# Optimization experiments

Hardware: AMD Instinct MI355X
Metric: run time of the kernel (lower is better)

## Reference

```python
import jax, jax.numpy as jnp
import numpy as np
import math

ALPHAS = [0.5, 1.0]
LSTM_SIZE = 512
LSTM_LAYERS = 2
OUTPUT_SIZE = 1024
INPUT_SIZE = 250


def _inv_gamma(z):
    # 1/gamma(z); gamma has poles at non-positive integers -> 1/gamma = 0 (matches scipy: gamma(0)=inf)
    if z <= 0 and float(z) == int(z):
        return 0.0
    return 1.0 / math.gamma(z)


def _caputo(x, alpha):
    # x: (B, T, N). D[t] = coef * sum_{j<t} (x[t]-x[j]) * (t-j+1e-6)^(-alpha)
    T = x.shape[1]
    t = jnp.arange(T, dtype=jnp.float32)
    diff = t[:, None] - t[None, :]
    W = jnp.where(diff > 0, (jnp.abs(diff) + 1e-6) ** (-alpha), 0.0)  # (T, T) strictly lower triangular
    coef = _inv_gamma(1.0 - alpha)
    rowsum = W.sum(axis=1)  # (T,)
    # coef * (x[t] * sum_j W[t,j] - sum_j W[t,j] x[j])
    return coef * (x * rowsum[None, :, None] - jnp.einsum('tj,bjn->btn', W, x))


def _lstm_layer(x, Wih, Whh, bih, bhh):
    # x: (B, T, F); torch LSTM gate order i, f, g, o
    B = x.shape[0]
    H = Whh.shape[1]
    xW = jnp.einsum('btf,gf->btg', x, Wih) + bih + bhh  # (B, T, 4H)
    h0 = jnp.zeros((B, H), dtype=x.dtype)
    c0 = jnp.zeros((B, H), dtype=x.dtype)

    def step(carry, xt):
        h, c = carry
        gates = xt + h @ Whh.T
        i, f, g, o = jnp.split(gates, 4, axis=-1)
        i = jax.nn.sigmoid(i)
        f = jax.nn.sigmoid(f)
        g = jnp.tanh(g)
        o = jax.nn.sigmoid(o)
        c = f * c + i * g
        h = o * jnp.tanh(c)
        return (h, c), h

    _, hs = jax.lax.scan(step, (h0, c0), jnp.swapaxes(xW, 0, 1))  # hs: (T, B, H)
    return jnp.swapaxes(hs, 0, 1)


def setup_inputs() -> dict:
    key = jax.random.key(0)
    ks = jax.random.split(key, 12)
    B, T, N = 64, 512, INPUT_SIZE
    H = LSTM_SIZE
    F_in = N * len(ALPHAS)
    s0 = 1.0 / math.sqrt(H)
    inp = {
        'x': jax.random.normal(ks[0], (B, T, N), dtype=jnp.float32),
        'Wih0': jax.random.uniform(ks[1], (4 * H, F_in), minval=-s0, maxval=s0, dtype=jnp.float32),
        'Whh0': jax.random.uniform(ks[2], (4 * H, H), minval=-s0, maxval=s0, dtype=jnp.float32),
        'bih0': jax.random.uniform(ks[3], (4 * H,), minval=-s0, maxval=s0, dtype=jnp.float32),
        'bhh0': jax.random.uniform(ks[4], (4 * H,), minval=-s0, maxval=s0, dtype=jnp.float32),
        'Wih1': jax.random.uniform(ks[5], (4 * H, H), minval=-s0, maxval=s0, dtype=jnp.float32),
        'Whh1': jax.random.uniform(ks[6], (4 * H, H), minval=-s0, maxval=s0, dtype=jnp.float32),
        'bih1': jax.random.uniform(ks[7], (4 * H,), minval=-s0, maxval=s0, dtype=jnp.float32),
        'bhh1': jax.random.uniform(ks[8], (4 * H,), minval=-s0, maxval=s0, dtype=jnp.float32),
        'Wout': jax.random.uniform(ks[9], (OUTPUT_SIZE, H), minval=-s0, maxval=s0, dtype=jnp.float32),
        'bout': jax.random.uniform(ks[10], (OUTPUT_SIZE,), minval=-s0, maxval=s0, dtype=jnp.float32),
    }
    return inp


def reference(x, Wih0, Whh0, bih0, bhh0, Wih1, Whh1, bih1, bhh1, Wout, bout):
    feats = jnp.concatenate([_caputo(x, a) for a in ALPHAS], axis=2)  # (B, T, N*len(alphas))
    h = _lstm_layer(feats, Wih0, Whh0, bih0, bhh0)
    h = _lstm_layer(h, Wih1, Whh1, bih1, bhh1)
    last = h[:, -1, :]
    return jax.nn.relu(last @ Wout.T + bout)
```

## Files before the change

kernel.cpp:

```cpp
#include <hip/hip_runtime.h>
#include <cstddef>

#define BB 64
#define TT 512
#define NN 250
#define HH 512
#define NB (NN*BB)
#define HB (HH*BB)
#define K0 762
#define K1 1024

__device__ __forceinline__ float sigmoidf_(float x) { return 1.0f / (1.0f + expf(-x)); }

__global__ __launch_bounds__(256) void k_transpose(const float* __restrict__ x,
                                                   float* __restrict__ xT) {
    const int t = blockIdx.x;
    const int n = blockIdx.y * 4 + (threadIdx.x >> 6);
    const int b = threadIdx.x & 63;
    if (n < NN)
        xT[(size_t)t * NB + n * BB + b] = x[(size_t)b * (TT * NN) + t * NN + n];
}

__global__ __launch_bounds__(512) void k_wrow(float* __restrict__ w, float* __restrict__ rowsum) {
    __shared__ float sw[TT];
    const int d = threadIdx.x;
    const float wd = (d >= 1) ? (1.0f / sqrtf((float)d + 1e-6f)) : 0.0f;
    sw[d] = wd;
    w[d] = wd;
    __syncthreads();
    float s = 0.0f;
    for (int j = 1; j <= d; ++j) s += sw[j];
    rowsum[d] = s;
}

__global__ __launch_bounds__(256) void k_caputo(const float* __restrict__ xT,
                                                const float* __restrict__ w,
                                                const float* __restrict__ rowsum,
                                                float* __restrict__ featsT) {
    const float COEF = 0.5641895835477563f;
    const int t0 = blockIdx.x * 4;
    const int nb0 = blockIdx.y * 1024 + threadIdx.x;
    float acc[4][4];
#pragma unroll
    for (int a = 0; a < 4; ++a)
#pragma unroll
        for (int e = 0; e < 4; ++e) acc[a][e] = 0.0f;

    for (int j = 0; j < t0; ++j) {
        const float* xj = xT + (size_t)j * NB;
        const float wt0 = w[t0 - j];
        const float wt1 = w[t0 + 1 - j];
        const float wt2 = w[t0 + 2 - j];
        const float wt3 = w[t0 + 3 - j];
#pragma unroll
        for (int e = 0; e < 4; ++e) {
            const int nb = nb0 + e * 256;
            const float xv = (nb < NB) ? xj[nb] : 0.0f;
            acc[0][e] = fmaf(wt0, xv, acc[0][e]);
            acc[1][e] = fmaf(wt1, xv, acc[1][e]);
            acc[2][e] = fmaf(wt2, xv, acc[2][e]);
            acc[3][e] = fmaf(wt3, xv, acc[3][e]);
        }
    }
#pragma unroll
    for (int dj = 0; dj < 3; ++dj) {
        const int j = t0 + dj;
        const float* xj = xT + (size_t)j * NB;
#pragma unroll
        for (int e = 0; e < 4; ++e) {
            const int nb = nb0 + e * 256;
            const float xv = (nb < NB) ? xj[nb] : 0.0f;
#pragma unroll
            for (int tt = 0; tt < 4; ++tt)
                if (tt > dj) acc[tt][e] = fmaf(w[tt - dj], xv, acc[tt][e]);
        }
    }
#pragma unroll
    for (int tt = 0; tt < 4; ++tt) {
        const int t = t0 + tt;
        const float rs = rowsum[t];
        const float* xt = xT + (size_t)t * NB;
        float* ft = featsT + (size_t)t * NB;
#pragma unroll
        for (int e = 0; e < 4; ++e) {
            const int nb = nb0 + e * 256;
            if (nb < NB) ft[nb] = COEF * fmaf(xt[nb], rs, -acc[tt][e]);
        }
    }
}

__global__ __launch_bounds__(256) void k_wt(const float* __restrict__ Wih0,
                                            const float* __restrict__ Whh0,
                                            const float* __restrict__ Wih1,
                                            const float* __restrict__ Whh1,
                                            float* __restrict__ WT0b,
                                            float* __restrict__ WT1b) {
    const int total0 = 128 * K0 * 16;
    const int total1 = 128 * K1 * 16;
    const int stride = gridDim.x * 256;
    for (int idx = blockIdx.x * 256 + threadIdx.x; idx < total0; idx += stride) {
        const int r = idx & 15;
        const int k = (idx >> 4) % K0;
        const int bi = idx / (16 * K0);
        const int row = (r & 3) * HH + bi * 4 + (r >> 2);
        WT0b[idx] = (k < NN) ? Wih0[(size_t)row * 500 + k] : Whh0[(size_t)row * HH + (k - NN)];
    }
    for (int idx = blockIdx.x * 256 + threadIdx.x; idx < total1; idx += stride) {
        const int r = idx & 15;
        const int k = (idx >> 4) % K1;
        const int bi = idx / (16 * K1);
        const int row = (r & 3) * HH + bi * 4 + (r >> 2);
        WT1b[idx] = (k < HH) ? Wih1[(size_t)row * HH + k] : Whh1[(size_t)row * HH + (k - HH)];
    }
}

__global__ __launch_bounds__(1024, 4) void k_step3(
    const float* __restrict__ featsT,
    const float* __restrict__ WT0b, const float* __restrict__ WT1b,
    const float* __restrict__ bih0, const float* __restrict__ bhh0,
    const float* __restrict__ bih1, const float* __restrict__ bhh1,
    float* __restrict__ h0T, float* __restrict__ c0T,
    float* __restrict__ h1T, float* __restrict__ c1T, int s) {
    __shared__ float lds[16384];
    const int tid = threadIdx.x;
    const int b = tid & 63;
    const int wv = tid >> 6;
    const bool isL1 = (blockIdx.x >= 128);
    if (!isL1 && s >= TT) return;
    if (isL1 && s < 1) return;
    const int bi = isL1 ? (blockIdx.x - 128) : blockIdx.x;
    const int rd = (s + 1) & 1;
    const float* __restrict__ h0rd = h0T + (size_t)rd * HB;

    {
        const float* __restrict__ wsrc = isL1 ? (WT1b + (size_t)bi * (K1 * 16))
                                              : (WT0b + (size_t)bi * (K0 * 16));
        const int nflt = (isL1 ? K1 : K0) * 16;
        for (int i = tid * 4; i < nflt; i += 4096)
            *reinterpret_cast<float4*>(&lds[i]) = *reinterpret_cast<const float4*>(wsrc + i);
    }
    __syncthreads();

    float acc[16];
#pragma unroll
    for (int r = 0; r < 16; ++r) acc[r] = 0.0f;

#define FMA16(KIDX, VV)                                                        \
    {                                                                          \
        const float4* wl = reinterpret_cast<const float4*>(&lds[(KIDX) * 16]); \
        const float4 w0_ = wl[0], w1_ = wl[1], w2_ = wl[2], w3_ = wl[3];       \
        acc[0] = fmaf(w0_.x, (VV), acc[0]);  acc[1] = fmaf(w0_.y, (VV), acc[1]); \
        acc[2] = fmaf(w0_.z, (VV), acc[2]);  acc[3] = fmaf(w0_.w, (VV), acc[3]); \
        acc[4] = fmaf(w1_.x, (VV), acc[4]);  acc[5] = fmaf(w1_.y, (VV), acc[5]); \
        acc[6] = fmaf(w1_.z, (VV), acc[6]);  acc[7] = fmaf(w1_.w, (VV), acc[7]); \
        acc[8] = fmaf(w2_.x, (VV), acc[8]);  acc[9] = fmaf(w2_.y, (VV), acc[9]); \
        acc[10] = fmaf(w2_.z, (VV), acc[10]); acc[11] = fmaf(w2_.w, (VV), acc[11]); \
        acc[12] = fmaf(w3_.x, (VV), acc[12]); acc[13] = fmaf(w3_.y, (VV), acc[13]); \
        acc[14] = fmaf(w3_.z, (VV), acc[14]); acc[15] = fmaf(w3_.w, (VV), acc[15]); \
    }

    if (!isL1) {
        const int k0 = __builtin_amdgcn_readfirstlane(wv * 48);
        int k1 = k0 + 48; if (k1 > K0) k1 = K0;
        {
            const float* __restrict__ vf = featsT + (size_t)s * NB + b;
            const int e = (k1 < NN) ? k1 : NN;
#pragma unroll 4
            for (int k = k0; k < e; ++k) {
                const float vv = vf[(size_t)k * 64];
                FMA16(k, vv)
            }
        }
        {
            const float* __restrict__ vh = h0rd + b;
            const int st = (k0 > NN) ? k0 : NN;
#pragma unroll 4
            for (int k = st; k < k1; ++k) {
                const float vv = vh[(size_t)(k - NN) * 64];
                FMA16(k, vv)
            }
        }
    } else {
        const int k0 = __builtin_amdgcn_readfirstlane(wv * 64);
        if (k0 < HH) {
            const float* __restrict__ vh = h0rd + b;
#pragma unroll 4
            for (int kk = 0; kk < 64; ++kk) {
                const int k = k0 + kk;
                const float vv = vh[(size_t)k * 64];
                FMA16(k, vv)
            }
        } else {
            const float* __restrict__ vh = h1T + (size_t)rd * HB + b;
#pragma unroll 4
            for (int kk = 0; kk < 64; ++kk) {
                const int k = k0 + kk;
                const float vv = vh[(size_t)(k - HH) * 64];
                FMA16(k, vv)
            }
        }
    }
#undef FMA16

    __syncthreads();
#pragma unroll
    for (int r = 0; r < 16; ++r) lds[(wv * 16 + r) * 64 + b] = acc[r];
    __syncthreads();

    if (wv < 4) {
        const int hu = bi * 4 + wv;
        const float* __restrict__ bi_ = isL1 ? bih1 : bih0;
        const float* __restrict__ bh_ = isL1 ? bhh1 : bhh0;
        float g4[4];
#pragma unroll
        for (int g = 0; g < 4; ++g) {
            float sum = bi_[g * HH + hu] + bh_[g * HH + hu];
#pragma unroll
            for (int i = 0; i < 16; ++i) sum += lds[(i * 16 + wv * 4 + g) * 64 + b];
            g4[g] = sum;
        }
        const float gi = sigmoidf_(g4[0]);
        const float gf = sigmoidf_(g4[1]);
        const float gg = tanhf(g4[2]);
        const float go = sigmoidf_(g4[3]);
        float* __restrict__ cT = isL1 ? c1T : c0T;
        const float cp = cT[hu * 64 + b];
        const float cn = fmaf(gf, cp, gi * gg);
        cT[hu * 64 + b] = cn;
        float* __restrict__ hT = (isL1 ? h1T : h0T) + (size_t)(s & 1) * HB;
        hT[hu * 64 + b] = go * tanhf(cn);
    }
}

__global__ __launch_bounds__(256) void k_out(const float* __restrict__ h1T,
                                             const float* __restrict__ Wout,
                                             const float* __restrict__ bout,
                                             float* __restrict__ out) {
    const int o = blockIdx.x * 4 + (threadIdx.x >> 6);
    const int b = threadIdx.x & 63;
    float acc = 0.0f;
    const float* wrow = Wout + (size_t)o * HH;
    for (int k = 0; k < HH; k += 4) {
        const float4 wv = *reinterpret_cast<const float4*>(wrow + k);
        acc = fmaf(wv.x, h1T[(k + 0) * BB + b],
              fmaf(wv.y, h1T[(k + 1) * BB + b],
              fmaf(wv.z, h1T[(k + 2) * BB + b],
              fmaf(wv.w, h1T[(k + 3) * BB + b], acc))));
    }
    acc += bout[o];
    out[(size_t)b * 1024 + o] = fmaxf(acc, 0.0f);
}

extern "C" void kernel_launch(void* const* d_in, const int* in_sizes, int n_in,
                              void* d_out, int out_size, void* d_ws, size_t ws_size,
                              hipStream_t stream) {
    (void)in_sizes; (void)n_in; (void)out_size; (void)ws_size;
    const float* x    = (const float*)d_in[0];
    const float* Wih0 = (const float*)d_in[1];
    const float* Whh0 = (const float*)d_in[2];
    const float* bih0 = (const float*)d_in[3];
    const float* bhh0 = (const float*)d_in[4];
    const float* Wih1 = (const float*)d_in[5];
    const float* Whh1 = (const float*)d_in[6];
    const float* bih1 = (const float*)d_in[7];
    const float* bhh1 = (const float*)d_in[8];
    const float* Wout = (const float*)d_in[9];
    const float* bout = (const float*)d_in[10];

    float* ws     = (float*)d_ws;
    float* xT     = ws;
    float* WT0b   = ws;
    float* WT1b   = WT0b + (size_t)128 * K0 * 16;
    float* featsT = xT + (size_t)TT * NB;
    float* w      = featsT + (size_t)TT * NB;
    float* rowsum = w + TT;
    float* h0T    = rowsum + TT;
    float* c0T    = h0T + 2 * (size_t)HB;
    float* h1T    = c0T + (size_t)HB;
    float* c1T    = h1T + 2 * (size_t)HB;
    (void)c1T;

    hipMemsetAsync(h0T, 0, (size_t)6 * HB * sizeof(float), stream);

    k_transpose<<<dim3(TT, 63), 256, 0, stream>>>(x, xT);
    k_wrow<<<1, TT, 0, stream>>>(w, rowsum);
    k_caputo<<<dim3(TT / 4, 16), 256, 0, stream>>>(xT, w, rowsum, featsT);
    k_wt<<<512, 256, 0, stream>>>(Wih0, Whh0, Wih1, Whh1, WT0b, WT1b);

    for (int s = 0; s <= TT; ++s)
        k_step3<<<256, 1024, 0, stream>>>(featsT, WT0b, WT1b, bih0, bhh0, bih1, bhh1,
                                          h0T, c0T, h1T, c1T, s);

    k_out<<<256, 256, 0, stream>>>(h1T, Wout, bout, (float*)d_out);
}
```

Before: 7.117 ms.

## Replace per-step kernel launches with persistent cooperative kernel and tree grid barrier

The 513 per-timestep launches are folded into one cooperative persistent kernel. Each block now loads its weight slice into LDS once and keeps the biases in registers. Timesteps are separated by a two-level atomic grid barrier: leaf counters for groups of 8 blocks, then a root counter and generation flag. This removes launch overhead and the repeated weight reload per step, at the cost of spin-wait barrier latency and a requirement that all 256 blocks of 1024 threads are co-resident.

```diff
diff --git a/kernel.cpp b/kernel.cpp
--- a/kernel.cpp
+++ b/kernel.cpp
@@ -114,122 +114,159 @@
     }
 }
 
-__global__ __launch_bounds__(1024, 4) void k_step3(
+#define AGENT __HIP_MEMORY_SCOPE_AGENT
+
+__global__ __launch_bounds__(1024, 4) void k_persist(
     const float* __restrict__ featsT,
     const float* __restrict__ WT0b, const float* __restrict__ WT1b,
     const float* __restrict__ bih0, const float* __restrict__ bhh0,
     const float* __restrict__ bih1, const float* __restrict__ bhh1,
     float* __restrict__ h0T, float* __restrict__ c0T,
-    float* __restrict__ h1T, float* __restrict__ c1T, int s) {
-    __shared__ float lds[16384];
+    float* __restrict__ h1T, float* __restrict__ c1T,
+    unsigned* __restrict__ bar) {
+    __shared__ float wlds[16384];
+    __shared__ float part[16384];
     const int tid = threadIdx.x;
     const int b = tid & 63;
     const int wv = tid >> 6;
-    const bool isL1 = (blockIdx.x >= 128);
-    if (!isL1 && s >= TT) return;
-    if (isL1 && s < 1) return;
-    const int bi = isL1 ? (blockIdx.x - 128) : blockIdx.x;
-    const int rd = (s + 1) & 1;
-    const float* __restrict__ h0rd = h0T + (size_t)rd * HB;
+    const int bid = blockIdx.x;
+    const bool isL1 = (bid >= 128);
+    const int bi = isL1 ? (bid - 128) : bid;
+
+    unsigned* leaf = bar + (bid >> 3) * 32;
+    unsigned* ggen = bar + 1024 + (bid >> 3) * 32;
+    unsigned* root = bar + 2048;
+    unsigned* gen  = bar + 2080;
 
     {
         const float* __restrict__ wsrc = isL1 ? (WT1b + (size_t)bi * (K1 * 16))
                                               : (WT0b + (size_t)bi * (K0 * 16));
         const int nflt = (isL1 ? K1 : K0) * 16;
         for (int i = tid * 4; i < nflt; i += 4096)
-            *reinterpret_cast<float4*>(&lds[i]) = *reinterpret_cast<const float4*>(wsrc + i);
-    }
-    __syncthreads();
-
-    float acc[16];
-#pragma unroll
-    for (int r = 0; r < 16; ++r) acc[r] = 0.0f;
-
-#define FMA16(KIDX, VV)                                                        \
-    {                                                                          \
-        const float4* wl = reinterpret_cast<const float4*>(&lds[(KIDX) * 16]); \
-        const float4 w0_ = wl[0], w1_ = wl[1], w2_ = wl[2], w3_ = wl[3];       \
-        acc[0] = fmaf(w0_.x, (VV), acc[0]);  acc[1] = fmaf(w0_.y, (VV), acc[1]); \
-        acc[2] = fmaf(w0_.z, (VV), acc[2]);  acc[3] = fmaf(w0_.w, (VV), acc[3]); \
-        acc[4] = fmaf(w1_.x, (VV), acc[4]);  acc[5] = fmaf(w1_.y, (VV), acc[5]); \
-        acc[6] = fmaf(w1_.z, (VV), acc[6]);  acc[7] = fmaf(w1_.w, (VV), acc[7]); \
-        acc[8] = fmaf(w2_.x, (VV), acc[8]);  acc[9] = fmaf(w2_.y, (VV), acc[9]); \
-        acc[10] = fmaf(w2_.z, (VV), acc[10]); acc[11] = fmaf(w2_.w, (VV), acc[11]); \
-        acc[12] = fmaf(w3_.x, (VV), acc[12]); acc[13] = fmaf(w3_.y, (VV), acc[13]); \
-        acc[14] = fmaf(w3_.z, (VV), acc[14]); acc[15] = fmaf(w3_.w, (VV), acc[15]); \
-    }
-
-    if (!isL1) {
-        const int k0 = __builtin_amdgcn_readfirstlane(wv * 48);
-        int k1 = k0 + 48; if (k1 > K0) k1 = K0;
-        {
-            const float* __restrict__ vf = featsT + (size_t)s * NB + b;
-            const int e = (k1 < NN) ? k1 : NN;
-#pragma unroll 4
-            for (int k = k0; k < e; ++k) {
-                const float vv = vf[(size_t)k * 64];
-                FMA16(k, vv)
-            }
-        }
-        {
-            const float* __restrict__ vh = h0rd + b;
-            const int st = (k0 > NN) ? k0 : NN;
-#pragma unroll 4
-            for (int k = st; k < k1; ++k) {
-                const float vv = vh[(size_t)(k - NN) * 64];
-                FMA16(k, vv)
-            }
-        }
-    } else {
-        const int k0 = __builtin_amdgcn_readfirstlane(wv * 64);
-        if (k0 < HH) {
-            const float* __restrict__ vh = h0rd + b;
-#pragma unroll 4
-            for (int kk = 0; kk < 64; ++kk) {
-                const int k = k0 + kk;
-                const float vv = vh[(size_t)k * 64];
-                FMA16(k, vv)
-            }
-        } else {
-            const float* __restrict__ vh = h1T + (size_t)rd * HB + b;
-#pragma unroll 4
-            for (int kk = 0; kk < 64; ++kk) {
-                const int k = k0 + kk;
-                const float vv = vh[(size_t)(k - HH) * 64];
-                FMA16(k, vv)
-            }
-        }
-    }
-#undef FMA16
-
-    __syncthreads();
-#pragma unroll
-    for (int r = 0; r < 16; ++r) lds[(wv * 16 + r) * 64 + b] = acc[r];
-    __syncthreads();
-
+            *reinterpret_cast<float4*>(&wlds[i]) = *reinterpret_cast<const float4*>(wsrc + i);
+    }
+    float bsum[4] = {0.f, 0.f, 0.f, 0.f};
     if (wv < 4) {
         const int hu = bi * 4 + wv;
         const float* __restrict__ bi_ = isL1 ? bih1 : bih0;
         const float* __restrict__ bh_ = isL1 ? bhh1 : bhh0;
-        float g4[4];
-#pragma unroll
-        for (int g = 0; g < 4; ++g) {
-            float sum = bi_[g * HH + hu] + bh_[g * HH + hu];
-#pragma unroll
-            for (int i = 0; i < 16; ++i) sum += lds[(i * 16 + wv * 4 + g) * 64 + b];
-            g4[g] = sum;
-        }
-        const float gi = sigmoidf_(g4[0]);
-        const float gf = sigmoidf_(g4[1]);
-        const float gg = tanhf(g4[2]);
-        const float go = sigmoidf_(g4[3]);
-        float* __restrict__ cT = isL1 ? c1T : c0T;
-        const float cp = cT[hu * 64 + b];
-        const float cn = fmaf(gf, cp, gi * gg);
-        cT[hu * 64 + b] = cn;
-        float* __restrict__ hT = (isL1 ? h1T : h0T) + (size_t)(s & 1) * HB;
-        hT[hu * 64 + b] = go * tanhf(cn);
-    }
+#pragma unroll
+        for (int g = 0; g < 4; ++g) bsum[g] = bi_[g * HH + hu] + bh_[g * HH + hu];
+    }
+    __syncthreads();
+
+#define FMA16(KIDX, VV)                                                         \
+    {                                                                           \
+        const float4* wl = reinterpret_cast<const float4*>(&wlds[(KIDX) * 16]); \
+        const float4 w0_ = wl[0], w1_ = wl[1], w2_ = wl[2], w3_ = wl[3];        \
+        acc[0] = fmaf(w0_.x, (VV), acc[0]);   acc[1] = fmaf(w0_.y, (VV), acc[1]);  \
+        acc[2] = fmaf(w0_.z, (VV), acc[2]);   acc[3] = fmaf(w0_.w, (VV), acc[3]);  \
+        acc[4] = fmaf(w1_.x, (VV), acc[4]);   acc[5] = fmaf(w1_.y, (VV), acc[5]);  \
+        acc[6] = fmaf(w1_.z, (VV), acc[6]);   acc[7] = fmaf(w1_.w, (VV), acc[7]);  \
+        acc[8] = fmaf(w2_.x, (VV), acc[8]);   acc[9] = fmaf(w2_.y, (VV), acc[9]);  \
+        acc[10] = fmaf(w2_.z, (VV), acc[10]); acc[11] = fmaf(w2_.w, (VV), acc[11]); \
+        acc[12] = fmaf(w3_.x, (VV), acc[12]); acc[13] = fmaf(w3_.y, (VV), acc[13]); \
+        acc[14] = fmaf(w3_.z, (VV), acc[14]); acc[15] = fmaf(w3_.w, (VV), acc[15]); \
+    }
+
+    for (int s = 0; s <= TT; ++s) {
+        const bool active = isL1 ? (s >= 1) : (s < TT);
+        if (active) {
+            const int rd = (s + 1) & 1;
+            const float* __restrict__ h0rd = h0T + (size_t)rd * HB;
+            float acc[16];
+#pragma unroll
+            for (int r = 0; r < 16; ++r) acc[r] = 0.0f;
+
+            if (!isL1) {
+                const int k0 = wv * 48;
+                int k1 = k0 + 48; if (k1 > K0) k1 = K0;
+                {
+                    const float* __restrict__ vf = featsT + (size_t)s * NB + b;
+                    const int e = (k1 < NN) ? k1 : NN;
+#pragma unroll 4
+                    for (int k = k0; k < e; ++k) {
+                        const float vv = vf[(size_t)k * 64];
+                        FMA16(k, vv)
+                    }
+                }
+                {
+                    const float* __restrict__ vh = h0rd + b;
+                    const int st = (k0 > NN) ? k0 : NN;
+#pragma unroll 4
+                    for (int k = st; k < k1; ++k) {
+                        const float vv = vh[(size_t)(k - NN) * 64];
+                        FMA16(k, vv)
+                    }
+                }
+            } else {
+                const int k0 = wv * 64;
+                if (k0 < HH) {
+                    const float* __restrict__ vh = h0rd + b;
+#pragma unroll 4
+                    for (int kk = 0; kk < 64; ++kk) {
+                        const int k = k0 + kk;
+                        const float vv = vh[(size_t)k * 64];
+                        FMA16(k, vv)
+                    }
+                } else {
+                    const float* __restrict__ vh = h1T + (size_t)rd * HB + b;
+#pragma unroll 4
+                    for (int kk = 0; kk < 64; ++kk) {
+                        const int k = k0 + kk;
+                        const float vv = vh[(size_t)(k - HH) * 64];
+                        FMA16(k, vv)
+                    }
+                }
+            }
+
+#pragma unroll
+            for (int r = 0; r < 16; ++r) part[(wv * 16 + r) * 64 + b] = acc[r];
+            __syncthreads();
+
+            if (wv < 4) {
+                float g4[4];
+#pragma unroll
+                for (int g = 0; g < 4; ++g) {
+                    float sum = bsum[g];
+#pragma unroll
+                    for (int i = 0; i < 16; ++i) sum += part[(i * 16 + wv * 4 + g) * 64 + b];
+                    g4[g] = sum;
+                }
+                const float gi = sigmoidf_(g4[0]);
+                const float gf = sigmoidf_(g4[1]);
+                const float gg = tanhf(g4[2]);
+                const float go = sigmoidf_(g4[3]);
+                const int hu = bi * 4 + wv;
+                float* __restrict__ cT = isL1 ? c1T : c0T;
+                const float cp = cT[hu * 64 + b];
+                const float cn = fmaf(gf, cp, gi * gg);
+                cT[hu * 64 + b] = cn;
+                float* __restrict__ hT = (isL1 ? h1T : h0T) + (size_t)(s & 1) * HB;
+                hT[hu * 64 + b] = go * tanhf(cn);
+            }
+        }
+        __syncthreads();
+        if (tid == 0) {
+            const unsigned target = (unsigned)(s + 1);
+            if (__hip_atomic_fetch_add(leaf, 1u, __ATOMIC_ACQ_REL, AGENT) == 7u) {
+                __hip_atomic_store(leaf, 0u, __ATOMIC_RELAXED, AGENT);
+                if (__hip_atomic_fetch_add(root, 1u, __ATOMIC_ACQ_REL, AGENT) == 31u) {
+                    __hip_atomic_store(root, 0u, __ATOMIC_RELAXED, AGENT);
+                    __hip_atomic_fetch_add(gen, 1u, __ATOMIC_ACQ_REL, AGENT);
+                } else {
+                    while (__hip_atomic_load(gen, __ATOMIC_ACQUIRE, AGENT) < target)
+                        __builtin_amdgcn_s_sleep(1);
+                }
+                __hip_atomic_fetch_add(ggen, 1u, __ATOMIC_ACQ_REL, AGENT);
+            } else {
+                while (__hip_atomic_load(ggen, __ATOMIC_ACQUIRE, AGENT) < target)
+                    __builtin_amdgcn_s_sleep(1);
+            }
+        }
+        __syncthreads();
+    }
+#undef FMA16
 }
 
 __global__ __launch_bounds__(256) void k_out(const float* __restrict__ h1T,
@@ -278,18 +315,20 @@
     float* c0T    = h0T + 2 * (size_t)HB;
     float* h1T    = c0T + (size_t)HB;
     float* c1T    = h1T + 2 * (size_t)HB;
-    (void)c1T;
+    unsigned* bar = (unsigned*)(c1T + (size_t)HB);
 
     hipMemsetAsync(h0T, 0, (size_t)6 * HB * sizeof(float), stream);
+    hipMemsetAsync(bar, 0, 4096 * sizeof(unsigned), stream);
 
     k_transpose<<<dim3(TT, 63), 256, 0, stream>>>(x, xT);
     k_wrow<<<1, TT, 0, stream>>>(w, rowsum);
     k_caputo<<<dim3(TT / 4, 16), 256, 0, stream>>>(xT, w, rowsum, featsT);
     k_wt<<<512, 256, 0, stream>>>(Wih0, Whh0, Wih1, Whh1, WT0b, WT1b);
 
-    for (int s = 0; s <= TT; ++s)
-        k_step3<<<256, 1024, 0, stream>>>(featsT, WT0b, WT1b, bih0, bhh0, bih1, bhh1,
-                                          h0T, c0T, h1T, c1T, s);
+    void* args[] = {(void*)&featsT, (void*)&WT0b, (void*)&WT1b,
+                    (void*)&bih0, (void*)&bhh0, (void*)&bih1, (void*)&bhh1,
+                    (void*)&h0T, (void*)&c0T, (void*)&h1T, (void*)&c1T, (void*)&bar};
+    hipLaunchCooperativeKernel((void*)k_persist, dim3(256), dim3(1024), args, 0, stream);
 
     k_out<<<256, 256, 0, stream>>>(h1T, Wout, bout, (float*)d_out);
 }
```

Measured after the change: 24.58 ms. 245% more time.
